# Kernel tuning notes

Measured on AMD Instinct MI355X. Metric: run time of the kernel, lower is better.

Reference implementation:

```python
import jax, jax.numpy as jnp
import numpy as np

SEQ_LEN = 256
VOCAB = 50000
EMBED = 300
PROJ = 200
ATT = 200
CLS = 3
B = 128


def setup_inputs() -> dict:
    key = jax.random.key(0)
    ks = jax.random.split(key, 16)
    s = lambda d: 1.0 / np.sqrt(d)
    return {
        "x1": jax.random.randint(ks[0], (B, SEQ_LEN), 0, VOCAB, dtype=jnp.int32),
        "x2": jax.random.randint(ks[1], (B, SEQ_LEN), 0, VOCAB, dtype=jnp.int32),
        "emb": jax.random.normal(ks[2], (VOCAB, EMBED), jnp.float32),
        # intra-attention forward_product FC (shared for x1/x2 via AUTO_REUSE)
        "Wi": jax.random.normal(ks[3], (EMBED, ATT), jnp.float32) * s(EMBED),
        "bi": jnp.zeros((ATT,), jnp.float32),
        "b_dist": jax.random.normal(ks[4], (1,), jnp.float32) * 0.1,
        # embed-scope projection (input is concat[x, xp] -> 2*EMBED), linear
        "Wp": jax.random.normal(ks[5], (2 * EMBED, PROJ), jnp.float32) * s(2 * EMBED),
        "bp": jnp.zeros((PROJ,), jnp.float32),
        # attent forward_product FC (shared)
        "Wa": jax.random.normal(ks[6], (PROJ, ATT), jnp.float32) * s(PROJ),
        "ba": jnp.zeros((ATT,), jnp.float32),
        # compare FC (shared, dim = input dim = 2*PROJ)
        "Wc": jax.random.normal(ks[7], (2 * PROJ, 2 * PROJ), jnp.float32) * s(2 * PROJ),
        "bc": jnp.zeros((2 * PROJ,), jnp.float32),
        # aggregate FC -> class logits (linear)
        "Wg": jax.random.normal(ks[8], (4 * PROJ, CLS), jnp.float32) * s(4 * PROJ),
        "bg": jnp.zeros((CLS,), jnp.float32),
    }


def _seq_mask(x):
    # tf.count_nonzero + tf.sequence_mask -> [B, L, 1] float mask
    size = jnp.sum((x != 0).astype(jnp.float32), axis=1)  # [B]
    m = (jnp.arange(SEQ_LEN)[None, :] < size[:, None]).astype(jnp.float32)
    return m[:, :, None]


def _intra(x, Wi, bi, b_dist):
    # forward_product on (x, x): relu FC then bilinear product -> [B, L, L]
    f = jax.nn.relu(x @ Wi + bi)
    att = jnp.einsum("bid,bjd->bij", f, f)
    idx = jnp.arange(SEQ_LEN)
    dist = jnp.abs(idx[None, :] - idx[:, None])
    bias = b_dist[0] * (dist >= 10).astype(jnp.float32)  # [L, L]
    xp = jnp.einsum("bik,bkj->bij", jax.nn.softmax(att + bias[None], axis=2), x)
    return jnp.concatenate([x, xp], axis=2)  # [B, L, 2*EMBED]


def reference(x1, x2, emb, Wi, bi, b_dist, Wp, bp, Wa, ba, Wc, bc, Wg, bg):
    mask1, mask2 = _seq_mask(x1), _seq_mask(x2)  # [B, L, 1]

    # embedding lookup with L2-normalized table
    emb_n = emb / jnp.linalg.norm(emb, axis=1, keepdims=True)
    e1, e2 = emb_n[x1], emb_n[x2]  # [B, L, EMBED]

    # intra-attention (distance-biased self alignment), doubles feature dim
    h1 = _intra(e1, Wi, bi, b_dist)
    h2 = _intra(e2, Wi, bi, b_dist)

    # linear projection to PROJ
    p1 = h1 @ Wp + bp  # [B, L, PROJ]
    p2 = h2 @ Wp + bp

    # attent: forward_product sim + mask + dual-axis softmax alignments
    a1 = jax.nn.relu(p1 @ Wa + ba)
    a2 = jax.nn.relu(p2 @ Wa + ba)
    sim = jnp.einsum("bid,bjd->bij", a1, a2)  # [B, L, L]
    sim = sim * (mask1 * jnp.swapaxes(mask2, 1, 2))
    alpha = jnp.einsum("bki,bkj->bij", jax.nn.softmax(sim, axis=1), p1)
    beta = jnp.einsum("bik,bkj->bij", jax.nn.softmax(sim, axis=2), p2)

    # compare (shared relu FC)
    v1 = jax.nn.relu(jnp.concatenate([p1, beta], 2) @ Wc + bc)
    v2 = jax.nn.relu(jnp.concatenate([p2, alpha], 2) @ Wc + bc)

    # aggregate: masked sum pooling + linear classifier
    v1 = jnp.sum(v1 * mask1, axis=1)  # [B, 2*PROJ]
    v2 = jnp.sum(v2 * mask2, axis=1)
    return jnp.concatenate([v1, v2], 1) @ Wg + bg  # [B, CLS]
```

## Files before the change

### kernel.cpp

```cpp
#include <hip/hip_runtime.h>
#include <math.h>

#define LSEQ 256
#define NB   128

typedef unsigned short u16;
typedef unsigned int   u32;
typedef __attribute__((ext_vector_type(8))) short bf16x8;
typedef __attribute__((ext_vector_type(4))) float f32x4;

static __device__ __forceinline__ u16 f2bf(float x) {
    union { float f; u32 u; } v; v.f = x;
    const u32 r = v.u + 0x7fffu + ((v.u >> 16) & 1u);
    return (u16)(r >> 16);
}
static __device__ __forceinline__ void glds16(const u16* src, u16* dst) {
    __builtin_amdgcn_global_load_lds(
        (const __attribute__((address_space(1))) u32*)src,
        (__attribute__((address_space(3))) u32*)dst, 16, 0, 0);
}

template<int EPI, bool BIAS, bool RELU>
__global__ __launch_bounds__(512)
void gemm(const u16* __restrict__ A, int lda,
          const u16* __restrict__ B, int ldb,
          u16* __restrict__ C, int ldc,
          const float* __restrict__ bias, int Nbias,
          float* __restrict__ pool, const float* __restrict__ pmask,
          int K, int Nwrite)
{
    __shared__ u16 As[128 * 64];
    __shared__ u16 Bs[256 * 64];

    const int m0 = blockIdx.y * 128;
    const int n0 = blockIdx.x * 256;
    const int t = threadIdx.x;
    const int lane = t & 63;
    const int w = t >> 6;
    const int wm = w >> 2;
    const int wn = w & 3;
    const int lr = lane & 15;
    const int lg = lane >> 4;

    f32x4 acc[4][4] = {};

    for (int k0 = 0; k0 < K; k0 += 64) {
#pragma unroll
        for (int i = 0; i < 2; ++i) {
            const int ch = w * 2 + i;
            const int row = (ch << 3) + (lane >> 3);
            const int slot = (lane & 7) ^ (row & 7);
            glds16(A + (long long)(m0 + row) * lda + k0 + (slot << 3), &As[ch << 9]);
        }
#pragma unroll
        for (int i = 0; i < 4; ++i) {
            const int ch = w * 4 + i;
            const int row = (ch << 3) + (lane >> 3);
            const int slot = (lane & 7) ^ (row & 7);
            glds16(B + (long long)(n0 + row) * ldb + k0 + (slot << 3), &Bs[ch << 9]);
        }
        __syncthreads();
#pragma unroll
        for (int kk = 0; kk < 2; ++kk) {
            bf16x8 af[4], bf[4];
#pragma unroll
            for (int mi = 0; mi < 4; ++mi) {
                const int row = wm * 64 + mi * 16 + lr;
                const int slot = ((kk << 2) + lg) ^ (row & 7);
                af[mi] = *reinterpret_cast<const bf16x8*>(&As[row * 64 + (slot << 3)]);
            }
#pragma unroll
            for (int ni = 0; ni < 4; ++ni) {
                const int row = wn * 64 + ni * 16 + lr;
                const int slot = ((kk << 2) + lg) ^ (row & 7);
                bf[ni] = *reinterpret_cast<const bf16x8*>(&Bs[row * 64 + (slot << 3)]);
            }
#pragma unroll
            for (int mi = 0; mi < 4; ++mi)
#pragma unroll
                for (int ni = 0; ni < 4; ++ni)
                    acc[mi][ni] = __builtin_amdgcn_mfma_f32_16x16x32_bf16(
                        af[mi], bf[ni], acc[mi][ni], 0, 0, 0);
        }
        __syncthreads();
    }

    const int rbase = lg << 2;
    if (EPI == 0) {
#pragma unroll
        for (int ni = 0; ni < 4; ++ni) {
            const int gc = n0 + wn * 64 + ni * 16 + lr;
            if (gc >= Nwrite) continue;
            float bcv = 0.f;
            if (BIAS) bcv = (gc < Nbias) ? bias[gc] : 0.f;
#pragma unroll
            for (int mi = 0; mi < 4; ++mi) {
#pragma unroll
                for (int r = 0; r < 4; ++r) {
                    const long long gr = m0 + wm * 64 + mi * 16 + rbase + r;
                    float x = acc[mi][ni][r];
                    if (BIAS) x += bcv;
                    if (RELU) x = fmaxf(x, 0.f);
                    C[gr * ldc + gc] = f2bf(x);
                }
            }
        }
    } else {
        __syncthreads();
        float* pool_s = reinterpret_cast<float*>(As);
        for (int i = t; i < 256; i += 512) pool_s[i] = 0.f;
        __syncthreads();
        const int b_lin = m0 >> 8;
        const int side  = b_lin >> 7;
        const int bb    = b_lin & 127;
        const float* mk = pmask + b_lin * 256 + (m0 & 255);
        float mrow[4][4];
#pragma unroll
        for (int mi = 0; mi < 4; ++mi)
#pragma unroll
            for (int r = 0; r < 4; ++r)
                mrow[mi][r] = mk[wm * 64 + mi * 16 + rbase + r];
#pragma unroll
        for (int ni = 0; ni < 4; ++ni) {
            const int lc = wn * 64 + ni * 16 + lr;
            const int gc = n0 + lc;
            const float bcv = (BIAS && gc < Nbias) ? bias[gc] : 0.f;
            float cs = 0.f;
#pragma unroll
            for (int mi = 0; mi < 4; ++mi)
#pragma unroll
                for (int r = 0; r < 4; ++r)
                    cs += fmaxf(acc[mi][ni][r] + bcv, 0.f) * mrow[mi][r];
            cs += __shfl_xor(cs, 16, 64);
            cs += __shfl_xor(cs, 32, 64);
            if (lg == 0) atomicAdd(&pool_s[lc], cs);
        }
        __syncthreads();
        for (int i = t; i < 256; i += 512) {
            const int gc = n0 + i;
            if (gc < Nwrite) atomicAdd(&pool[bb * 800 + side * 400 + gc], pool_s[i]);
        }
    }
}

template<int MODE>
__global__ __launch_bounds__(512)
void fattn(const u16* __restrict__ QK, u16* __restrict__ Hb,
           u16* __restrict__ CMP, u16* __restrict__ CMP2,
           const float* __restrict__ M1, const float* __restrict__ M2,
           const float* __restrict__ b_dist)
{
    constexpr int NVT = (MODE == 0) ? 5 : 4;
    __shared__ char shmem[57344];
    u16* Ks = (u16*)shmem;
    u16* Qs = (u16*)(shmem + 32768);
    float* red  = (float*)(shmem + 49152);
    float* red2 = (float*)(shmem + 51200);
    u16* Pc = (u16*)shmem;
    u16* Vc = (u16*)(shmem + 16384);

    const int bz = blockIdx.x;
    int b, half, rowoff, ldv, ldc, Nwrite;
    const u16 *Kp, *Qp, *Vp;
    u16* Cp;
    const float *mrow = nullptr, *mcol = nullptr;
    if (MODE == 0) {
        b = (bz & 7) + (bz >> 4) * 8;
        half = (bz >> 3) & 1;
        Kp = QK + (long long)b * 65536;
        Qp = Kp;
        Vp = Hb + (long long)b * 163840; ldv = 640;
        Cp = Hb + (long long)b * 163840 + half * 128 * 640 + 320;
        ldc = 640; Nwrite = 320; rowoff = half * 128;
    } else {
        const int xcd = bz & 7, j = bz >> 3;
        const int sib = j & 3;
        b = xcd + (j >> 2) * 8;
        half = sib & 1;
        const int v = sib >> 1;
        const u16* a1 = QK + (long long)b * 65536;
        const u16* a2 = QK + 32768LL * 256 + (long long)b * 65536;
        u16* P1 = CMP  + (long long)b * 114688;
        u16* P2 = CMP2 + (long long)b * 114688;
        if (v == 0) { Qp = a1 + half * 128 * 256; Kp = a2; Vp = P2;
                      Cp = P1 + half * 128 * 448 + 200;
                      mrow = M1 + b * 256 + half * 128; mcol = M2 + b * 256; }
        else        { Qp = a2 + half * 128 * 256; Kp = a1; Vp = P1;
                      Cp = P2 + half * 128 * 448 + 200;
                      mrow = M2 + b * 256 + half * 128; mcol = M1 + b * 256; }
        ldv = 448; ldc = 448; Nwrite = 248; rowoff = 0;
    }

    const int t = threadIdx.x, lane = t & 63, w = t >> 6;
    const int lr = lane & 15, lg = lane >> 4;
    const int wk = w >> 1, wr = w & 1;
    const int wr2 = w >> 2, wc = w & 3;

    f32x4 acc[4][4] = {};
    for (int k0 = 0; k0 < 256; k0 += 64) {
#pragma unroll
        for (int i = 0; i < 4; ++i) {
            const int ch = w * 4 + i;
            const int row = (ch << 3) + (lane >> 3);
            const int slot = (lane & 7) ^ (row & 7);
            glds16(Kp + (long long)row * 256 + k0 + (slot << 3), &Ks[ch << 9]);
        }
        if (MODE != 0) {
#pragma unroll
            for (int i = 0; i < 2; ++i) {
                const int ch = w * 2 + i;
                const int row = (ch << 3) + (lane >> 3);
                const int slot = (lane & 7) ^ (row & 7);
                glds16(Qp + (long long)row * 256 + k0 + (slot << 3), &Qs[ch << 9]);
            }
        }
        __syncthreads();
#pragma unroll
        for (int kk = 0; kk < 2; ++kk) {
            bf16x8 kf[4], qf[4];
#pragma unroll
            for (int ki = 0; ki < 4; ++ki) {
                const int row = wk * 64 + ki * 16 + lr;
                const int slot = ((kk << 2) + lg) ^ (row & 7);
                kf[ki] = *reinterpret_cast<const bf16x8*>(&Ks[row * 64 + (slot << 3)]);
            }
#pragma unroll
            for (int qi = 0; qi < 4; ++qi) {
                if (MODE == 0) {
                    const int row = rowoff + wr * 64 + qi * 16 + lr;
                    const int slot = ((kk << 2) + lg) ^ (row & 7);
                    qf[qi] = *reinterpret_cast<const bf16x8*>(&Ks[row * 64 + (slot << 3)]);
                } else {
                    const int row = wr * 64 + qi * 16 + lr;
                    const int slot = ((kk << 2) + lg) ^ (row & 7);
                    qf[qi] = *reinterpret_cast<const bf16x8*>(&Qs[row * 64 + (slot << 3)]);
                }
            }
#pragma unroll
            for (int ki = 0; ki < 4; ++ki)
#pragma unroll
                for (int qi = 0; qi < 4; ++qi)
                    acc[ki][qi] = __builtin_amdgcn_mfma_f32_16x16x32_bf16(
                        kf[ki], qf[qi], acc[ki][qi], 0, 0, 0);
        }
        __syncthreads();
    }

    if (MODE == 1) {
        float mr[4], mc[4][4];
#pragma unroll
        for (int qi = 0; qi < 4; ++qi) mr[qi] = mrow[wr * 64 + qi * 16 + lr];
#pragma unroll
        for (int ki = 0; ki < 4; ++ki)
#pragma unroll
            for (int r = 0; r < 4; ++r)
                mc[ki][r] = mcol[wk * 64 + ki * 16 + (lg << 2) + r];
#pragma unroll
        for (int ki = 0; ki < 4; ++ki)
#pragma unroll
            for (int qi = 0; qi < 4; ++qi)
#pragma unroll
                for (int r = 0; r < 4; ++r)
                    acc[ki][qi][r] *= mr[qi] * mc[ki][r];
    } else {
        const float bd = b_dist[0];
#pragma unroll
        for (int ki = 0; ki < 4; ++ki)
#pragma unroll
            for (int qi = 0; qi < 4; ++qi)
#pragma unroll
                for (int r = 0; r < 4; ++r) {
                    const int irow = rowoff + wr * 64 + qi * 16 + lr;
                    const int jcol = wk * 64 + ki * 16 + (lg << 2) + r;
                    const int d = irow > jcol ? irow - jcol : jcol - irow;
                    if (d >= 10) acc[ki][qi][r] += bd;
                }
    }

    const int n4  = (t & 63) << 2;
    const int k8v = (t >> 6) << 3;
    const int n4b = 256 + ((t & 15) << 2);
    const int k8b = (t >> 4) << 3;
    uint2 vreg[8], vtail[8];
#pragma unroll
    for (int i = 0; i < 8; ++i)
        vreg[i] = *reinterpret_cast<const uint2*>(Vp + (long long)(k8v + i) * ldv + n4);
    if (NVT == 5) {
        if (t < 128) {
#pragma unroll
            for (int i = 0; i < 8; ++i)
                vtail[i] = *reinterpret_cast<const uint2*>(Vp + (long long)(k8b + i) * ldv + n4b);
        }
    }

    float mx[4];
#pragma unroll
    for (int qi = 0; qi < 4; ++qi) {
        float m_ = -1e30f;
#pragma unroll
        for (int ki = 0; ki < 4; ++ki)
#pragma unroll
            for (int r = 0; r < 4; ++r) m_ = fmaxf(m_, acc[ki][qi][r]);
        m_ = fmaxf(m_, __shfl_xor(m_, 16, 64));
        m_ = fmaxf(m_, __shfl_xor(m_, 32, 64));
        mx[qi] = m_;
    }
    if (lg == 0) {
#pragma unroll
        for (int qi = 0; qi < 4; ++qi)
            red[(wr * 64 + qi * 16 + lr) * 4 + wk] = mx[qi];
    }
    __syncthreads();
    float sm[4];
#pragma unroll
    for (int qi = 0; qi < 4; ++qi) {
        const int row = wr * 64 + qi * 16 + lr;
        const float m_ = fmaxf(fmaxf(red[row * 4 + 0], red[row * 4 + 1]),
                               fmaxf(red[row * 4 + 2], red[row * 4 + 3]));
        float s_ = 0.f;
#pragma unroll
        for (int ki = 0; ki < 4; ++ki)
#pragma unroll
            for (int r = 0; r < 4; ++r) {
                const float e_ = __expf(acc[ki][qi][r] - m_);
                acc[ki][qi][r] = e_;
                s_ += e_;
            }
        s_ += __shfl_xor(s_, 16, 64);
        s_ += __shfl_xor(s_, 32, 64);
        sm[qi] = s_;
    }
    if (lg == 0) {
#pragma unroll
        for (int qi = 0; qi < 4; ++qi)
            red2[(wr * 64 + qi * 16 + lr) * 4 + wk] = sm[qi];
    }
    __syncthreads();
#pragma unroll
    for (int qi = 0; qi < 4; ++qi) {
        const int row = wr * 64 + qi * 16 + lr;
        const float rs = 1.0f / (red2[row * 4 + 0] + red2[row * 4 + 1]
                               + red2[row * 4 + 2] + red2[row * 4 + 3]);
#pragma unroll
        for (int ki = 0; ki < 4; ++ki)
#pragma unroll
            for (int r = 0; r < 4; ++r) acc[ki][qi][r] *= rs;
    }
    __syncthreads();

    f32x4 opv[4][NVT] = {};
    for (int c = 0; c < 4; ++c) {
        {
            union { uint2 q2[8]; u16 s[32]; } uq;
#pragma unroll
            for (int i = 0; i < 8; ++i) uq.q2[i] = vreg[i];
#pragma unroll
            for (int j = 0; j < 4; ++j) {
                const int row = n4 + j;
                const u32 v0 = (u32)uq.s[j]      | ((u32)uq.s[4 + j]  << 16);
                const u32 v1 = (u32)uq.s[8 + j]  | ((u32)uq.s[12 + j] << 16);
                const u32 v2 = (u32)uq.s[16 + j] | ((u32)uq.s[20 + j] << 16);
                const u32 v3 = (u32)uq.s[24 + j] | ((u32)uq.s[28 + j] << 16);
                const int slot = (t >> 6) ^ (row & 7);
                *reinterpret_cast<uint4*>(&Vc[row * 64 + (slot << 3)]) =
                    make_uint4(v0, v1, v2, v3);
            }
            if (NVT == 5 && t < 128) {
                union { uint2 q2[8]; u16 s[32]; } ub;
#pragma unroll
                for (int i = 0; i < 8; ++i) ub.q2[i] = vtail[i];
#pragma unroll
                for (int j = 0; j < 4; ++j) {
                    const int row = n4b + j;
                    const u32 v0 = (u32)ub.s[j]      | ((u32)ub.s[4 + j]  << 16);
                    const u32 v1 = (u32)ub.s[8 + j]  | ((u32)ub.s[12 + j] << 16);
                    const u32 v2 = (u32)ub.s[16 + j] | ((u32)ub.s[20 + j] << 16);
                    const u32 v3 = (u32)ub.s[24 + j] | ((u32)ub.s[28 + j] << 16);
                    const int slot = (t >> 4) ^ (row & 7);
                    *reinterpret_cast<uint4*>(&Vc[row * 64 + (slot << 3)]) =
                        make_uint4(v0, v1, v2, v3);
                }
            }
        }
        if (wk == c) {
#pragma unroll
            for (int qi = 0; qi < 4; ++qi) {
                const int qrow = wr * 64 + qi * 16 + lr;
#pragma unroll
                for (int ki = 0; ki < 4; ++ki) {
                    const u32 lo = (u32)f2bf(acc[ki][qi][0]) | ((u32)f2bf(acc[ki][qi][1]) << 16);
                    const u32 hi = (u32)f2bf(acc[ki][qi][2]) | ((u32)f2bf(acc[ki][qi][3]) << 16);
                    const int slot = ((ki << 1) + (lg >> 1)) ^ (qrow & 7);
                    *reinterpret_cast<uint2*>(
                        (char*)Pc + qrow * 128 + (slot << 4) + ((lg & 1) << 3)) =
                        make_uint2(lo, hi);
                }
            }
        }
        if (c < 3) {
#pragma unroll
            for (int i = 0; i < 8; ++i)
                vreg[i] = *reinterpret_cast<const uint2*>(
                    Vp + (long long)((c + 1) * 64 + k8v + i) * ldv + n4);
            if (NVT == 5 && t < 128) {
#pragma unroll
                for (int i = 0; i < 8; ++i)
                    vtail[i] = *reinterpret_cast<const uint2*>(
                        Vp + (long long)((c + 1) * 64 + k8b + i) * ldv + n4b);
            }
        }
        __syncthreads();
#pragma unroll
        for (int kk = 0; kk < 2; ++kk) {
            bf16x8 pa[4], vb[NVT];
#pragma unroll
            for (int qi = 0; qi < 4; ++qi) {
                const int row = wr2 * 64 + qi * 16 + lr;
                const int slot = ((kk << 2) + lg) ^ (row & 7);
                pa[qi] = *reinterpret_cast<const bf16x8*>(&Pc[row * 64 + (slot << 3)]);
            }
#pragma unroll
            for (int vi = 0; vi < NVT; ++vi) {
                const int row = wc * (NVT * 16) + vi * 16 + lr;
                const int slot = ((kk << 2) + lg) ^ (row & 7);
                vb[vi] = *reinterpret_cast<const bf16x8*>(&Vc[row * 64 + (slot << 3)]);
            }
#pragma unroll
            for (int qi = 0; qi < 4; ++qi)
#pragma unroll
                for (int vi = 0; vi < NVT; ++vi)
                    opv[qi][vi] = __builtin_amdgcn_mfma_f32_16x16x32_bf16(
                        pa[qi], vb[vi], opv[qi][vi], 0, 0, 0);
        }
        __syncthreads();
    }

#pragma unroll
    for (int qi = 0; qi < 4; ++qi)
#pragma unroll
        for (int vi = 0; vi < NVT; ++vi) {
            const int gc = wc * (NVT * 16) + vi * 16 + lr;
            if (gc >= Nwrite) continue;
#pragma unroll
            for (int r = 0; r < 4; ++r) {
                const int qrow = wr2 * 64 + qi * 16 + (lg << 2) + r;
                Cp[(long long)qrow * ldc + gc] = f2bf(opv[qi][vi][r]);
            }
        }
}

__global__ __launch_bounds__(256)
void prep_small(const int* __restrict__ x1, const int* __restrict__ x2,
                float* __restrict__ M1f, float* __restrict__ POOL)
{
    const int blk = blockIdx.x;
    const int b = blk & 127;
    const int t = threadIdx.x;
    const int* x = (blk < 128) ? x1 : x2;
    float* mask = M1f + (blk < 128 ? 0 : 32768);
    int nz = (x[b * LSEQ + t] != 0) ? 1 : 0;
#pragma unroll
    for (int o = 32; o; o >>= 1) nz += __shfl_xor(nz, o, 64);
    __shared__ int red[4];
    if ((t & 63) == 0) red[t >> 6] = nz;
    __syncthreads();
    const int size = red[0] + red[1] + red[2] + red[3];
    mask[b * LSEQ + t] = (t < size) ? 1.0f : 0.0f;
    if (blk < 128) {
        for (int i = t; i < 800; i += 256) POOL[b * 800 + i] = 0.f;
    }
}

__global__ __launch_bounds__(256)
void prep_weights(const float* __restrict__ Wi, const float* __restrict__ Wa,
                  const float* __restrict__ Wp, const float* __restrict__ Wc,
                  u16* __restrict__ WiT, u16* __restrict__ WaT,
                  u16* __restrict__ WpT, u16* __restrict__ WcT)
{
    int idx = blockIdx.x * 256 + threadIdx.x;
    const float* src; u16* dst; int srcRows, srcCols, dstCols, seg1, seg2;
    if (idx < 81920)       { src = Wi; dst = WiT; srcRows = 300; srcCols = 200; dstCols = 320; seg1 = 300; seg2 = 320; }
    else if (idx < 147456) { idx -= 81920;  src = Wa; dst = WaT; srcRows = 200; srcCols = 200; dstCols = 256; seg1 = 200; seg2 = 256; }
    else if (idx < 311296) { idx -= 147456; src = Wp; dst = WpT; srcRows = 600; srcCols = 200; dstCols = 640; seg1 = 300; seg2 = 320; }
    else                   { idx -= 311296; src = Wc; dst = WcT; srcRows = 400; srcCols = 400; dstCols = 448; seg1 = 400; seg2 = 448; }
    const int n = idx / dstCols, k = idx - n * dstCols;
    int sr = -1;
    if (k < seg1) sr = k;
    else if (k >= seg2 && (k - seg2) < (srcRows - seg1)) sr = seg1 + (k - seg2);
    u16 v = 0;
    if (n < srcCols && sr >= 0) v = f2bf(src[(long long)sr * srcCols + n]);
    dst[idx] = v;
}

__global__ __launch_bounds__(256)
void gather_norm(const int* __restrict__ x1, const int* __restrict__ x2,
                 const float* __restrict__ emb, u16* __restrict__ h)
{
    const int t = threadIdx.x;
    const int lane = t & 63;
    const long long row = (long long)blockIdx.x * 4 + (t >> 6);
    const int tok = (row < 32768) ? x1[row] : x2[row - 32768];
    const float* er = emb + (long long)tok * 300;
    float vals[5];
    float ss = 0.f;
#pragma unroll
    for (int i = 0; i < 5; ++i) {
        const int c = lane + i * 64;
        const float v = (c < 300) ? er[c] : 0.f;
        vals[i] = v;
        ss = fmaf(v, v, ss);
    }
#pragma unroll
    for (int o = 32; o; o >>= 1) ss += __shfl_xor(ss, o, 64);
    const float inv = 1.0f / sqrtf(ss);
    u16* out = h + row * 640;
#pragma unroll
    for (int i = 0; i < 5; ++i) {
        const int c = lane + i * 64;
        out[c] = f2bf(vals[i] * inv);
    }
}

__global__ __launch_bounds__(256)
void final_fc(const float* __restrict__ pooled, const float* __restrict__ Wg,
              const float* __restrict__ bg, float* __restrict__ out)
{
    const int b = blockIdx.x;
    const int t = threadIdx.x;
    float a0 = 0.f, a1 = 0.f, a2 = 0.f;
    for (int k = t; k < 800; k += 256) {
        const float p = pooled[(long long)b * 800 + k];
        a0 = fmaf(p, Wg[k * 3 + 0], a0);
        a1 = fmaf(p, Wg[k * 3 + 1], a1);
        a2 = fmaf(p, Wg[k * 3 + 2], a2);
    }
#pragma unroll
    for (int o = 32; o; o >>= 1) {
        a0 += __shfl_xor(a0, o, 64);
        a1 += __shfl_xor(a1, o, 64);
        a2 += __shfl_xor(a2, o, 64);
    }
    __shared__ float r0[4], r1[4], r2[4];
    if ((t & 63) == 0) { r0[t >> 6] = a0; r1[t >> 6] = a1; r2[t >> 6] = a2; }
    __syncthreads();
    if (t == 0) {
        out[b * 3 + 0] = r0[0] + r0[1] + r0[2] + r0[3] + bg[0];
        out[b * 3 + 1] = r1[0] + r1[1] + r1[2] + r1[3] + bg[1];
        out[b * 3 + 2] = r2[0] + r2[1] + r2[2] + r2[3] + bg[2];
    }
}

extern "C" void kernel_launch(void* const* d_in, const int* in_sizes, int n_in,
                              void* d_out, int out_size, void* d_ws, size_t ws_size,
                              hipStream_t stream)
{
    (void)in_sizes; (void)n_in; (void)out_size; (void)ws_size;

    const int*   x1     = (const int*)  d_in[0];
    const int*   x2     = (const int*)  d_in[1];
    const float* emb    = (const float*)d_in[2];
    const float* Wi     = (const float*)d_in[3];
    const float* bi     = (const float*)d_in[4];
    const float* b_dist = (const float*)d_in[5];
    const float* Wp     = (const float*)d_in[6];
    const float* bp     = (const float*)d_in[7];
    const float* Wa     = (const float*)d_in[8];
    const float* ba     = (const float*)d_in[9];
    const float* Wc     = (const float*)d_in[10];
    const float* bc     = (const float*)d_in[11];
    const float* Wg     = (const float*)d_in[12];
    const float* bg     = (const float*)d_in[13];
    float* out = (float*)d_out;

    u16* wsu  = (u16*)d_ws;
    u16* H    = wsu;
    u16* CMP  = wsu + 41943040;
    u16* FA   = wsu + 71303168;
    u16* WiT  = wsu + 88080384;
    u16* WaT  = wsu + 88162304;
    u16* WpT  = wsu + 88227840;
    u16* WcT  = wsu + 88391680;
    float* fb = (float*)(wsu + 88621056);
    float* POOL = fb;
    float* M1f  = fb + 102400;
    float* M2f  = fb + 135168;

    u16* CMP2 = CMP + (long long)32768 * 448;

    prep_small<<<256, 256, 0, stream>>>(x1, x2, M1f, POOL);
    prep_weights<<<2112, 256, 0, stream>>>(Wi, Wa, Wp, Wc, WiT, WaT, WpT, WcT);
    gather_norm<<<16384, 256, 0, stream>>>(x1, x2, emb, H);

    gemm<0, true, true><<<dim3(1, 512, 1), 512, 0, stream>>>(
        H, 640, WiT, 320, FA, 256, bi, 200, nullptr, nullptr, 320, 256);
    fattn<0><<<512, 512, 0, stream>>>(FA, H, nullptr, nullptr, nullptr, nullptr, b_dist);
    gemm<0, true, false><<<dim3(1, 512, 1), 512, 0, stream>>>(
        H, 640, WpT, 640, CMP, 448, bp, 200, nullptr, nullptr, 640, 256);
    gemm<0, true, true><<<dim3(1, 512, 1), 512, 0, stream>>>(
        CMP, 448, WaT, 256, FA, 256, ba, 200, nullptr, nullptr, 256, 256);
    fattn<1><<<512, 512, 0, stream>>>(FA, nullptr, CMP, CMP2, M1f, M2f, nullptr);
    gemm<2, true, true><<<dim3(2, 512, 1), 512, 0, stream>>>(
        CMP, 448, WcT, 448, nullptr, 0, bc, 400, POOL, M1f, 448, 400);

    final_fc<<<NB, 256, 0, stream>>>(POOL, Wg, bg, out);
}
```

Baseline: 207.9 us.

## Load QK^T operands directly from global memory and shrink LDS footprint

The score-GEMM stage of the fused attention kernel now reads its K and Q fragments straight from global memory into registers, replacing the staging through LDS with global_load_lds and the block barriers around it. The shared-memory buffer shrinks to what the P·V stage needs, with the reduction scratch aliased onto it, which could allow more resident blocks per CU. MFMA loops are also wrapped in s_setprio to raise wave priority during compute. The trade-off is that each wave now fetches overlapping K/Q tiles redundantly from global memory or cache, with less coalesced access than the staged copies.

```diff
diff --git a/kernel.cpp b/kernel.cpp
--- a/kernel.cpp
+++ b/kernel.cpp
@@ -151,13 +151,11 @@
            const float* __restrict__ b_dist)
 {
     constexpr int NVT = (MODE == 0) ? 5 : 4;
-    __shared__ char shmem[57344];
-    u16* Ks = (u16*)shmem;
-    u16* Qs = (u16*)(shmem + 32768);
-    float* red  = (float*)(shmem + 49152);
-    float* red2 = (float*)(shmem + 51200);
+    __shared__ __align__(16) char shmem[16384 + NVT * 8192];
     u16* Pc = (u16*)shmem;
     u16* Vc = (u16*)(shmem + 16384);
+    float* red  = (float*)shmem;
+    float* red2 = red + 512;
 
     const int bz = blockIdx.x;
     int b, half, rowoff, ldv, ldc, Nwrite;
@@ -168,10 +166,11 @@
         b = (bz & 7) + (bz >> 4) * 8;
         half = (bz >> 3) & 1;
         Kp = QK + (long long)b * 65536;
-        Qp = Kp;
+        rowoff = half * 128;
+        Qp = Kp + rowoff * 256;
         Vp = Hb + (long long)b * 163840; ldv = 640;
         Cp = Hb + (long long)b * 163840 + half * 128 * 640 + 320;
-        ldc = 640; Nwrite = 320; rowoff = half * 128;
+        ldc = 640; Nwrite = 320;
     } else {
         const int xcd = bz & 7, j = bz >> 3;
         const int sib = j & 3;
@@ -199,51 +198,26 @@
     f32x4 acc[4][4] = {};
     for (int k0 = 0; k0 < 256; k0 += 64) {
 #pragma unroll
-        for (int i = 0; i < 4; ++i) {
-            const int ch = w * 4 + i;
-            const int row = (ch << 3) + (lane >> 3);
-            const int slot = (lane & 7) ^ (row & 7);
-            glds16(Kp + (long long)row * 256 + k0 + (slot << 3), &Ks[ch << 9]);
-        }
-        if (MODE != 0) {
-#pragma unroll
-            for (int i = 0; i < 2; ++i) {
-                const int ch = w * 2 + i;
-                const int row = (ch << 3) + (lane >> 3);
-                const int slot = (lane & 7) ^ (row & 7);
-                glds16(Qp + (long long)row * 256 + k0 + (slot << 3), &Qs[ch << 9]);
-            }
-        }
-        __syncthreads();
-#pragma unroll
         for (int kk = 0; kk < 2; ++kk) {
+            const int ko = k0 + kk * 32 + lg * 8;
             bf16x8 kf[4], qf[4];
 #pragma unroll
-            for (int ki = 0; ki < 4; ++ki) {
-                const int row = wk * 64 + ki * 16 + lr;
-                const int slot = ((kk << 2) + lg) ^ (row & 7);
-                kf[ki] = *reinterpret_cast<const bf16x8*>(&Ks[row * 64 + (slot << 3)]);
-            }
-#pragma unroll
-            for (int qi = 0; qi < 4; ++qi) {
-                if (MODE == 0) {
-                    const int row = rowoff + wr * 64 + qi * 16 + lr;
-                    const int slot = ((kk << 2) + lg) ^ (row & 7);
-                    qf[qi] = *reinterpret_cast<const bf16x8*>(&Ks[row * 64 + (slot << 3)]);
-                } else {
-                    const int row = wr * 64 + qi * 16 + lr;
-                    const int slot = ((kk << 2) + lg) ^ (row & 7);
-                    qf[qi] = *reinterpret_cast<const bf16x8*>(&Qs[row * 64 + (slot << 3)]);
-                }
-            }
+            for (int ki = 0; ki < 4; ++ki)
+                kf[ki] = *reinterpret_cast<const bf16x8*>(
+                    Kp + (long long)(wk * 64 + ki * 16 + lr) * 256 + ko);
+#pragma unroll
+            for (int qi = 0; qi < 4; ++qi)
+                qf[qi] = *reinterpret_cast<const bf16x8*>(
+                    Qp + (long long)(wr * 64 + qi * 16 + lr) * 256 + ko);
+            __builtin_amdgcn_s_setprio(1);
 #pragma unroll
             for (int ki = 0; ki < 4; ++ki)
 #pragma unroll
                 for (int qi = 0; qi < 4; ++qi)
                     acc[ki][qi] = __builtin_amdgcn_mfma_f32_16x16x32_bf16(
                         kf[ki], qf[qi], acc[ki][qi], 0, 0, 0);
-        }
-        __syncthreads();
+            __builtin_amdgcn_s_setprio(0);
+        }
     }
 
     if (MODE == 1) {
@@ -425,12 +399,14 @@
                 const int slot = ((kk << 2) + lg) ^ (row & 7);
                 vb[vi] = *reinterpret_cast<const bf16x8*>(&Vc[row * 64 + (slot << 3)]);
             }
+            __builtin_amdgcn_s_setprio(1);
 #pragma unroll
             for (int qi = 0; qi < 4; ++qi)
 #pragma unroll
                 for (int vi = 0; vi < NVT; ++vi)
                     opv[qi][vi] = __builtin_amdgcn_mfma_f32_16x16x32_bf16(
                         pa[qi], vb[vi], opv[qi][vi], 0, 0, 0);
+            __builtin_amdgcn_s_setprio(0);
         }
         __syncthreads();
     }
```

New measurement: 244.8 us. 17.8% more time.
